# Performance work log

Hardware: AMD Instinct MI355X
Metric: run time of the kernel (lower is better)

## Reference

```python
import jax, jax.numpy as jnp
import numpy as np

DECAY = 0.95     # importance_decay
BUDGET = 1.0     # attention_budget
TOP_K = 10       # recall top_k used by get_context_embedding
EPS = 1e-8


def _gelu(x):
    # torch nn.GELU default = exact erf variant
    return jax.nn.gelu(x, approximate=False)


def setup_inputs() -> dict:
    key = jax.random.key(0)
    ks = jax.random.split(key, 8)
    B, N, D, H = 4096, 100, 4096, 128
    query = jax.random.normal(ks[0], (B, D), dtype=jnp.float32)
    seg_emb = jax.random.normal(ks[1], (N, D), dtype=jnp.float32)
    positions = jnp.arange(N, dtype=jnp.int32)
    s1 = 1.0 / np.sqrt(D)
    s2 = 1.0 / np.sqrt(H)
    iw1 = jax.random.normal(ks[2], (D, H), dtype=jnp.float32) * s1
    ib1 = jnp.zeros((H,), dtype=jnp.float32)
    iw2 = jax.random.normal(ks[3], (H, 1), dtype=jnp.float32) * s2
    ib2 = jnp.zeros((1,), dtype=jnp.float32)
    rw1 = jax.random.normal(ks[4], (2 * D, H), dtype=jnp.float32) * (1.0 / np.sqrt(2 * D))
    rb1 = jnp.zeros((H,), dtype=jnp.float32)
    rw2 = jax.random.normal(ks[5], (H, 1), dtype=jnp.float32) * s2
    rb2 = jnp.zeros((1,), dtype=jnp.float32)
    return {"query": query, "seg_emb": seg_emb, "positions": positions,
            "iw1": iw1, "ib1": ib1, "iw2": iw2, "ib2": ib2,
            "rw1": rw1, "rb1": rb1, "rw2": rw2, "rb2": rb2}


def reference(query, seg_emb, positions, iw1, ib1, iw2, ib2, rw1, rb1, rw2, rb2):
    # query: [B, D], seg_emb: [N, D]
    B, D = query.shape
    N = seg_emb.shape[0]

    # importance_scorer per segment: Linear->GELU->Linear->Sigmoid, [N]
    importance = jax.nn.sigmoid(_gelu(seg_emb @ iw1 + ib1) @ iw2 + ib2)[:, 0]

    # relevance_scorer on concat([query, seg]); split rw1 to avoid [B,N,2D] concat
    qh = query @ rw1[:D]            # [B, H]
    sh = seg_emb @ rw1[D:]          # [N, H]
    h = _gelu(qh[:, None, :] + sh[None, :, :] + rb1)   # [B, N, H]
    rel = jax.nn.sigmoid(jnp.einsum('bnh,ho->bn', h, rw2) + rb2[0])  # [B, N]

    # recall score: importance * relevance * (0.5 + 0.5 * decay^(N - pos - 1))
    pos_factor = DECAY ** (N - positions.astype(jnp.float32) - 1.0)  # [N]
    score = importance[None, :] * rel * (0.5 + 0.5 * pos_factor[None, :])

    _, topi = jax.lax.top_k(score, TOP_K)               # [B, K]

    sel_rel = jnp.take_along_axis(rel, topi, axis=1)    # [B, K]
    sel_imp = importance[topi]                          # [B, K]
    w = sel_imp * sel_rel
    w = w / (jnp.sum(w, axis=-1, keepdims=True) + EPS) * BUDGET

    sel_emb = seg_emb[topi]                             # [B, K, D]
    context = jnp.einsum('bk,bkd->bd', w, sel_emb)      # [B, D]
    return query + context
```

## Files before the change

kernel.cpp:

```cpp
#include <hip/hip_runtime.h>
#include <math.h>

#define DDIM 4096
#define NSEG 100
#define HDIM 128
#define BROWS 4096
#define TOPK 10
#define KSLICES 8

typedef __attribute__((ext_vector_type(8))) short bf16x8;
typedef __attribute__((ext_vector_type(4))) float f32x4;

__device__ __forceinline__ void gl16(const void* g, void* l) {
    __builtin_amdgcn_global_load_lds(
        (const __attribute__((address_space(1))) unsigned int*)g,
        (__attribute__((address_space(3))) unsigned int*)l,
        16, 0, 0);
}

__device__ __forceinline__ float gelu_f(float x) {
    float u  = x * 0.70710678118654752440f;
    float au = fminf(fabsf(u), 3.9f);
    float t  = __builtin_amdgcn_rcpf(fmaf(0.3275911f, au, 1.0f));
    float p  = fmaf(fmaf(fmaf(fmaf(1.061405429f, t, -1.453152027f), t,
                              1.421413741f), t, -0.284496736f), t, 0.254829592f) * t;
    float e  = __expf(-au * au);
    float er = fmaf(-p, e, 1.0f);
    er = copysignf(er, u);
    return 0.5f * x * (1.0f + er);
}

__device__ __forceinline__ void split8(const float4& a, const float4& b,
                                       bf16x8& hi, bf16x8& lo) {
    float v[8] = {a.x, a.y, a.z, a.w, b.x, b.y, b.z, b.w};
    uint hw[4], lw[4];
    #pragma unroll
    for (int j = 0; j < 4; ++j) {
        uint u0 = __float_as_uint(v[2 * j]);
        uint u1 = __float_as_uint(v[2 * j + 1]);
        hw[j] = (u0 >> 16) | (u1 & 0xffff0000u);
        float r0 = v[2 * j]     - __uint_as_float(u0 & 0xffff0000u);
        float r1 = v[2 * j + 1] - __uint_as_float(u1 & 0xffff0000u);
        lw[j] = (__float_as_uint(r0) >> 16) | (__float_as_uint(r1) & 0xffff0000u);
    }
    uint4 h = make_uint4(hw[0], hw[1], hw[2], hw[3]);
    uint4 l = make_uint4(lw[0], lw[1], lw[2], lw[3]);
    hi = __builtin_bit_cast(bf16x8, h);
    lo = __builtin_bit_cast(bf16x8, l);
}

__global__ void k_front(const float* __restrict__ seg,
                        const float* __restrict__ iw1,
                        const float* __restrict__ rw1,
                        float* __restrict__ segp,
                        unsigned char* __restrict__ btI) {
    __shared__ __align__(16) float shf[32 * 129];
    int bid = blockIdx.x, tid = threadIdx.x;
    if (bid < 1600) {
        float (*segT)[5] = reinterpret_cast<float (*)[5]>(shf);
        int ng = bid % 25;
        int ks = (bid / 25) * 64;
        {
            int k = tid & 63, j = tid >> 6;
            segT[k][j] = seg[(size_t)(ng * 4 + j) * DDIM + ks + k];
        }
        __syncthreads();
        int col = tid;
        float a0 = 0.f, a1 = 0.f, a2 = 0.f, a3 = 0.f;
        const float* w = (col < HDIM) ? (iw1 + col)
                                      : (rw1 + (size_t)DDIM * HDIM + (col - HDIM));
        #pragma unroll 8
        for (int k = 0; k < 64; ++k) {
            float wv = w[(size_t)(ks + k) * HDIM];
            a0 = fmaf(segT[k][0], wv, a0);
            a1 = fmaf(segT[k][1], wv, a1);
            a2 = fmaf(segT[k][2], wv, a2);
            a3 = fmaf(segT[k][3], wv, a3);
        }
        float* outp = segp + (size_t)(bid / 25) * (NSEG * 256) + (size_t)(ng * 4) * 256 + col;
        outp[0] = a0; outp[256] = a1; outp[512] = a2; outp[768] = a3;
    } else {
        float (*tile)[129] = reinterpret_cast<float (*)[129]>(shf);
        int c = bid - 1600;
        #pragma unroll
        for (int i = 0; i < 4; ++i) {
            int e = i * 1024 + tid * 4;
            int k = e >> 7, n = e & 127;
            *reinterpret_cast<float4*>(&tile[k][n]) =
                *reinterpret_cast<const float4*>(rw1 + (size_t)(c * 32 + k) * HDIM + n);
        }
        __syncthreads();
        unsigned char* img = btI + (size_t)c * 16384;
        #pragma unroll
        for (int uu = 0; uu < 2; ++uu) {
            int U = tid * 2 + uu;
            int col = U >> 2;
            int u = U & 3;
            int Z = (col * 64 + u * 16) ^ ((col & 7) << 4);
            uint hw[4], lw[4];
            #pragma unroll
            for (int j = 0; j < 4; ++j) {
                float x0 = tile[u * 8 + 2 * j][col];
                float x1 = tile[u * 8 + 2 * j + 1][col];
                uint u0 = __float_as_uint(x0), u1 = __float_as_uint(x1);
                hw[j] = (u0 >> 16) | (u1 & 0xffff0000u);
                float r0 = x0 - __uint_as_float(u0 & 0xffff0000u);
                float r1 = x1 - __uint_as_float(u1 & 0xffff0000u);
                lw[j] = (__float_as_uint(r0) >> 16) | (__float_as_uint(r1) & 0xffff0000u);
            }
            *reinterpret_cast<uint4*>(img + Z)        = make_uint4(hw[0], hw[1], hw[2], hw[3]);
            *reinterpret_cast<uint4*>(img + 8192 + Z) = make_uint4(lw[0], lw[1], lw[2], lw[3]);
        }
    }
}

__global__ __launch_bounds__(256)
void k_mid(const float* __restrict__ query,
           const unsigned char* __restrict__ btI,
           float* __restrict__ qhp,
           const float* __restrict__ segp,
           const int* __restrict__ positions,
           const float* __restrict__ ib1,
           const float* __restrict__ iw2,
           const float* __restrict__ ib2,
           const float* __restrict__ rb1,
           float* __restrict__ shwT, float* __restrict__ impA,
           float* __restrict__ cA) {
    __shared__ __align__(16) char lds[49152];
    int bid = blockIdx.x, tid = threadIdx.x;
    if (bid < 512) {
        float  (*Ab)[2048] = reinterpret_cast<float (*)[2048]>(lds);
        ushort (*Bb)[8192] = reinterpret_cast<ushort (*)[8192]>(lds + 16384);
        int lane = tid & 63, w = tid >> 6;
        int cl = lane & 15, rg = lane >> 4;
        int wm = w >> 1, wn = w & 1;
        int m0 = (bid & 63) * 64;
        int ky = bid >> 6;
        int k0 = ky * 512;

        const float* aSrc0;
        const float* aSrc1;
        {
            int X0 = w * 2048 + lane * 16;
            int r0_ = X0 >> 7, kb0 = (X0 & 127) ^ ((r0_ & 7) << 4);
            aSrc0 = query + (size_t)(m0 + r0_) * DDIM + k0 + (kb0 >> 2);
            int X1 = X0 + 1024;
            int r1_ = X1 >> 7, kb1 = (X1 & 127) ^ ((r1_ & 7) << 4);
            aSrc1 = query + (size_t)(m0 + r1_) * DDIM + k0 + (kb1 >> 2);
        }
        const unsigned char* bSrc = btI + (size_t)(ky * 16) * 16384 + w * 4096 + lane * 16;

        f32x4 acc[2][4];
        #pragma unroll
        for (int mi = 0; mi < 2; ++mi)
            #pragma unroll
            for (int nf = 0; nf < 4; ++nf) acc[mi][nf] = (f32x4)0.f;

        {
            char* ad = (char*)&Ab[0][0] + w * 2048;
            char* bd = (char*)&Bb[0][0] + w * 4096;
            gl16(aSrc0, ad);
            gl16(aSrc1, ad + 1024);
            #pragma unroll
            for (int j = 0; j < 4; ++j) gl16(bSrc + j * 1024, bd + j * 1024);
        }
        __syncthreads();

        #pragma unroll 2
        for (int t = 0; t < 16; ++t) {
            int cur = t & 1;
            if (t < 15) {
                char* ad = (char*)&Ab[cur ^ 1][0] + w * 2048;
                char* bd = (char*)&Bb[cur ^ 1][0] + w * 4096;
                gl16(aSrc0 + (t + 1) * 32, ad);
                gl16(aSrc1 + (t + 1) * 32, ad + 1024);
                const unsigned char* bs = bSrc + (size_t)(t + 1) * 16384;
                #pragma unroll
                for (int j = 0; j < 4; ++j) gl16(bs + j * 1024, bd + j * 1024);
            }
            bf16x8 ah[2], al[2];
            #pragma unroll
            for (int mi = 0; mi < 2; ++mi) {
                int row = wm * 32 + mi * 16 + cl;
                int sw = (row & 7) << 4;
                int Sb = row * 128 + rg * 32;
                float4 f0 = *reinterpret_cast<const float4*>((const char*)&Ab[cur][0] + (Sb ^ sw));
                float4 f1 = *reinterpret_cast<const float4*>((const char*)&Ab[cur][0] + ((Sb + 16) ^ sw));
                split8(f0, f1, ah[mi], al[mi]);
            }
            #pragma unroll
            for (int nf = 0; nf < 4; ++nf) {
                int col = wn * 64 + nf * 16 + cl;
                int Z = (col * 64 + rg * 16) ^ ((col & 7) << 4);
                bf16x8 bh = *reinterpret_cast<const bf16x8*>((const char*)&Bb[cur][0] + Z);
                bf16x8 bl = *reinterpret_cast<const bf16x8*>((const char*)&Bb[cur][0] + 8192 + Z);
                #pragma unroll
                for (int mi = 0; mi < 2; ++mi) {
                    acc[mi][nf] = __builtin_amdgcn_mfma_f32_16x16x32_bf16(ah[mi], bh, acc[mi][nf], 0, 0, 0);
                    acc[mi][nf] = __builtin_amdgcn_mfma_f32_16x16x32_bf16(al[mi], bh, acc[mi][nf], 0, 0, 0);
                    acc[mi][nf] = __builtin_amdgcn_mfma_f32_16x16x32_bf16(ah[mi], bl, acc[mi][nf], 0, 0, 0);
                }
            }
            __syncthreads();
        }

        float* op = qhp + (size_t)ky * (BROWS * HDIM);
        #pragma unroll
        for (int mi = 0; mi < 2; ++mi) {
            int rowb = m0 + wm * 32 + mi * 16 + rg * 4;
            #pragma unroll
            for (int nf = 0; nf < 4; ++nf) {
                int col = wn * 64 + nf * 16 + cl;
                #pragma unroll
                for (int r = 0; r < 4; ++r)
                    op[(size_t)(rowb + r) * HDIM + col] = acc[mi][nf][r];
            }
        }
    } else {
        float* red = reinterpret_cast<float*>(lds);
        int n = bid - 512;
        float v = 0.f;
        #pragma unroll
        for (int s = 0; s < 64; ++s)
            v += segp[(size_t)s * (NSEG * 256) + (size_t)n * 256 + tid];
        if (tid < HDIM) {
            red[tid] = gelu_f(v + ib1[tid]) * iw2[tid];
        } else {
            shwT[(size_t)(tid - HDIM) * NSEG + n] = v + rb1[tid - HDIM];
        }
        __syncthreads();
        if (tid == 0) {
            float s = 0.f;
            for (int j = 0; j < HDIM; ++j) s += red[j];
            float imp = 1.f / (1.f + expf(-(s + ib2[0])));
            float pf = powf(0.95f, (float)NSEG - (float)positions[n] - 1.0f);
            impA[n] = imp;
            cA[n] = imp * (0.5f + 0.5f * pf);
        }
    }
}

__global__ __launch_bounds__(256)
void k_relg(const float* __restrict__ qhp,
            const float* __restrict__ shwT,
            const float* __restrict__ rw2,
            const float* __restrict__ rb2,
            const float* __restrict__ impA,
            const float* __restrict__ cA,
            const float* __restrict__ query,
            const float* __restrict__ seg,
            float* __restrict__ out) {
    __shared__ float qs[2][HDIM];
    __shared__ float scL[2][128], wiL[2][128];
    __shared__ float wnS[2][TOPK];
    __shared__ int   idxS[2][TOPK];
    int tid = threadIdx.x;
    int b0 = blockIdx.x * 2;
    int g = tid >> 7, n = tid & 127;

    {
        size_t o = (size_t)(b0 + g) * HDIM + n;
        float v = qhp[o];
        #pragma unroll
        for (int s = 1; s < KSLICES; ++s)
            v += qhp[(size_t)s * (BROWS * HDIM) + o];
        qs[g][n] = v;
    }
    __syncthreads();

    int nn = (n < NSEG) ? n : (NSEG - 1);
    float a0 = 0.f;
    #pragma unroll 2
    for (int h = 0; h < HDIM; ++h) {
        float s = shwT[h * NSEG + nn];
        float w = rw2[h];
        a0 = fmaf(gelu_f(qs[g][h] + s), w, a0);
    }
    if (n < NSEG) {
        float rel = 1.f / (1.f + expf(-(a0 + rb2[0])));
        scL[g][n] = cA[n] * rel;
        wiL[g][n] = impA[n] * rel;
    }
    __syncthreads();

    int w = tid >> 6, lane = tid & 63;
    if (w < 2) {
        int rr = w;
        float s1 = scL[rr][lane];
        float w1 = wiL[rr][lane];
        int i2 = lane + 64;
        float s2 = (i2 < NSEG) ? scL[rr][i2] : -1e30f;
        float w2 = (i2 < NSEG) ? wiL[rr][i2] : 0.f;

        float wv[TOPK]; int idxv[TOPK]; float wsum = 0.f;
        #pragma unroll
        for (int k = 0; k < TOPK; ++k) {
            float s; int i;
            if (s2 > s1) { s = s2; i = i2; } else { s = s1; i = lane; }
            #pragma unroll
            for (int off = 1; off < 64; off <<= 1) {
                float os = __shfl_xor(s, off);
                int oi = __shfl_xor(i, off);
                if (os > s || (os == s && oi < i)) { s = os; i = oi; }
            }
            float wi = __shfl((i < 64) ? w1 : w2, i & 63);
            idxv[k] = i; wv[k] = wi; wsum += wi;
            if (i == lane) s1 = -1e30f;
            if (i == i2)   s2 = -1e30f;
        }
        if (lane == 0) {
            float denom = wsum + 1e-8f;
            #pragma unroll
            for (int k = 0; k < TOPK; ++k) {
                idxS[rr][k] = idxv[k];
                wnS[rr][k]  = wv[k] / denom;
            }
        }
    }
    __syncthreads();

    #pragma unroll
    for (int r = 0; r < 2; ++r) {
        int b = b0 + r;
        float wn_[TOPK]; const float* srow[TOPK];
        #pragma unroll
        for (int k = 0; k < TOPK; ++k) {
            wn_[k]  = wnS[r][k];
            srow[k] = seg + (size_t)idxS[r][k] * DDIM;
        }
        const float* qrow = query + (size_t)b * DDIM;
        float* orow = out + (size_t)b * DDIM;
        #pragma unroll
        for (int c = 0; c < 4; ++c) {
            int d0 = c * 1024 + tid * 4;
            float4 q4 = *reinterpret_cast<const float4*>(qrow + d0);
            #pragma unroll
            for (int k = 0; k < TOPK; ++k) {
                float4 s4 = *reinterpret_cast<const float4*>(srow[k] + d0);
                q4.x = fmaf(wn_[k], s4.x, q4.x);
                q4.y = fmaf(wn_[k], s4.y, q4.y);
                q4.z = fmaf(wn_[k], s4.z, q4.z);
                q4.w = fmaf(wn_[k], s4.w, q4.w);
            }
            *reinterpret_cast<float4*>(orow + d0) = q4;
        }
    }
}

extern "C" void kernel_launch(void* const* d_in, const int* in_sizes, int n_in,
                              void* d_out, int out_size, void* d_ws, size_t ws_size,
                              hipStream_t stream) {
    const float* query = (const float*)d_in[0];
    const float* seg   = (const float*)d_in[1];
    const int*   pos   = (const int*)d_in[2];
    const float* iw1   = (const float*)d_in[3];
    const float* ib1   = (const float*)d_in[4];
    const float* iw2   = (const float*)d_in[5];
    const float* ib2   = (const float*)d_in[6];
    const float* rw1   = (const float*)d_in[7];
    const float* rb1   = (const float*)d_in[8];
    const float* rw2   = (const float*)d_in[9];
    const float* rb2   = (const float*)d_in[10];
    float* out = (float*)d_out;

    char* ws = (char*)d_ws;
    float* qhp  = (float*)(ws);
    float* segp = (float*)(ws + 16 * 1024 * 1024);
    unsigned char* btI = (unsigned char*)(ws + 23 * 1024 * 1024);
    float* shwT = (float*)(ws + 25 * 1024 * 1024);
    float* impA = (float*)(ws + 25 * 1024 * 1024 + 64 * 1024);
    float* cA   = (float*)(ws + 25 * 1024 * 1024 + 64 * 1024 + 4096);

    hipLaunchKernelGGL(k_front, dim3(1728), dim3(256), 0, stream,
                       seg, iw1, rw1, segp, btI);
    hipLaunchKernelGGL(k_mid, dim3(612), dim3(256), 0, stream,
                       query, btI, qhp, segp, pos, ib1, iw2, ib2, rb1,
                       shwT, impA, cA);
    hipLaunchKernelGGL(k_relg, dim3(BROWS / 2), dim3(256), 0, stream,
                       qhp, shwT, rw2, rb2, impA, cA, query, seg, out);
}
```

Baseline: 125.0 us.

## Split relevance/top-k and gather into separate kernels with more rows per block

The fused relevance+topk+gather kernel is split in two. The relevance kernel now handles 4 rows per block, each thread computes two rows sharing the shwT loads, and all four waves run top-k. It writes indices and normalized weights to workspace. A new gather kernel uses one block per row and issues all four float4 query loads plus per-k segment loads up front to get more memory-level parallelism. This adds a kernel launch and a small workspace round trip.

```diff
diff --git a/kernel.cpp b/kernel.cpp
--- a/kernel.cpp
+++ b/kernel.cpp
@@ -241,50 +241,55 @@
 }
 
 __global__ __launch_bounds__(256)
-void k_relg(const float* __restrict__ qhp,
-            const float* __restrict__ shwT,
-            const float* __restrict__ rw2,
-            const float* __restrict__ rb2,
-            const float* __restrict__ impA,
-            const float* __restrict__ cA,
-            const float* __restrict__ query,
-            const float* __restrict__ seg,
-            float* __restrict__ out) {
-    __shared__ float qs[2][HDIM];
-    __shared__ float scL[2][128], wiL[2][128];
-    __shared__ float wnS[2][TOPK];
-    __shared__ int   idxS[2][TOPK];
+void k_rel(const float* __restrict__ qhp,
+           const float* __restrict__ shwT,
+           const float* __restrict__ rw2,
+           const float* __restrict__ rb2,
+           const float* __restrict__ impA,
+           const float* __restrict__ cA,
+           int* __restrict__ idxA,
+           float* __restrict__ wnA) {
+    __shared__ float qs[4][HDIM];
+    __shared__ float scL[4][128], wiL[4][128];
     int tid = threadIdx.x;
-    int b0 = blockIdx.x * 2;
-    int g = tid >> 7, n = tid & 127;
-
-    {
-        size_t o = (size_t)(b0 + g) * HDIM + n;
+    int b0 = blockIdx.x * 4;
+
+    #pragma unroll
+    for (int i = 0; i < 2; ++i) {
+        int idx = tid + i * 256;
+        int r = idx >> 7, h = idx & 127;
+        size_t o = (size_t)(b0 + r) * HDIM + h;
         float v = qhp[o];
         #pragma unroll
         for (int s = 1; s < KSLICES; ++s)
             v += qhp[(size_t)s * (BROWS * HDIM) + o];
-        qs[g][n] = v;
+        qs[r][h] = v;
     }
     __syncthreads();
 
+    int g = tid >> 7, n = tid & 127;
     int nn = (n < NSEG) ? n : (NSEG - 1);
-    float a0 = 0.f;
+    int r0 = g * 2;
+    float a0 = 0.f, a1 = 0.f;
     #pragma unroll 2
     for (int h = 0; h < HDIM; ++h) {
         float s = shwT[h * NSEG + nn];
         float w = rw2[h];
-        a0 = fmaf(gelu_f(qs[g][h] + s), w, a0);
+        a0 = fmaf(gelu_f(qs[r0 + 0][h] + s), w, a0);
+        a1 = fmaf(gelu_f(qs[r0 + 1][h] + s), w, a1);
     }
     if (n < NSEG) {
-        float rel = 1.f / (1.f + expf(-(a0 + rb2[0])));
-        scL[g][n] = cA[n] * rel;
-        wiL[g][n] = impA[n] * rel;
+        float rb2f = rb2[0];
+        float ca = cA[n], ia = impA[n];
+        float rel0 = 1.f / (1.f + expf(-(a0 + rb2f)));
+        float rel1 = 1.f / (1.f + expf(-(a1 + rb2f)));
+        scL[r0 + 0][n] = ca * rel0;  wiL[r0 + 0][n] = ia * rel0;
+        scL[r0 + 1][n] = ca * rel1;  wiL[r0 + 1][n] = ia * rel1;
     }
     __syncthreads();
 
     int w = tid >> 6, lane = tid & 63;
-    if (w < 2) {
+    {
         int rr = w;
         float s1 = scL[rr][lane];
         float w1 = wiL[rr][lane];
@@ -309,42 +314,55 @@
             if (i == i2)   s2 = -1e30f;
         }
         if (lane == 0) {
+            int b = b0 + rr;
             float denom = wsum + 1e-8f;
             #pragma unroll
             for (int k = 0; k < TOPK; ++k) {
-                idxS[rr][k] = idxv[k];
-                wnS[rr][k]  = wv[k] / denom;
-            }
-        }
-    }
-    __syncthreads();
-
-    #pragma unroll
-    for (int r = 0; r < 2; ++r) {
-        int b = b0 + r;
-        float wn_[TOPK]; const float* srow[TOPK];
-        #pragma unroll
-        for (int k = 0; k < TOPK; ++k) {
-            wn_[k]  = wnS[r][k];
-            srow[k] = seg + (size_t)idxS[r][k] * DDIM;
-        }
-        const float* qrow = query + (size_t)b * DDIM;
-        float* orow = out + (size_t)b * DDIM;
+                idxA[b * TOPK + k] = idxv[k];
+                wnA[b * TOPK + k]  = wv[k] / denom;
+            }
+        }
+    }
+}
+
+__global__ void k_gather(const float* __restrict__ query,
+                         const float* __restrict__ seg,
+                         const int* __restrict__ idxA,
+                         const float* __restrict__ wnA,
+                         float* __restrict__ out) {
+    int b = blockIdx.x, tid = threadIdx.x;
+    const int*   ip = idxA + b * TOPK;
+    const float* wp = wnA  + b * TOPK;
+    float wn[TOPK]; const float* srow[TOPK];
+    #pragma unroll
+    for (int k = 0; k < TOPK; ++k) {
+        wn[k]   = wp[k];
+        srow[k] = seg + (size_t)ip[k] * DDIM;
+    }
+    const float* qrow = query + (size_t)b * DDIM;
+    float* orow = out + (size_t)b * DDIM;
+
+    float4 q[4];
+    #pragma unroll
+    for (int c = 0; c < 4; ++c)
+        q[c] = *reinterpret_cast<const float4*>(qrow + c * 1024 + tid * 4);
+    #pragma unroll
+    for (int k = 0; k < TOPK; ++k) {
+        float4 s[4];
+        #pragma unroll
+        for (int c = 0; c < 4; ++c)
+            s[c] = *reinterpret_cast<const float4*>(srow[k] + c * 1024 + tid * 4);
         #pragma unroll
         for (int c = 0; c < 4; ++c) {
-            int d0 = c * 1024 + tid * 4;
-            float4 q4 = *reinterpret_cast<const float4*>(qrow + d0);
-            #pragma unroll
-            for (int k = 0; k < TOPK; ++k) {
-                float4 s4 = *reinterpret_cast<const float4*>(srow[k] + d0);
-                q4.x = fmaf(wn_[k], s4.x, q4.x);
-                q4.y = fmaf(wn_[k], s4.y, q4.y);
-                q4.z = fmaf(wn_[k], s4.z, q4.z);
-                q4.w = fmaf(wn_[k], s4.w, q4.w);
-            }
-            *reinterpret_cast<float4*>(orow + d0) = q4;
-        }
-    }
+            q[c].x = fmaf(wn[k], s[c].x, q[c].x);
+            q[c].y = fmaf(wn[k], s[c].y, q[c].y);
+            q[c].z = fmaf(wn[k], s[c].z, q[c].z);
+            q[c].w = fmaf(wn[k], s[c].w, q[c].w);
+        }
+    }
+    #pragma unroll
+    for (int c = 0; c < 4; ++c)
+        *reinterpret_cast<float4*>(orow + c * 1024 + tid * 4) = q[c];
 }
 
 extern "C" void kernel_launch(void* const* d_in, const int* in_sizes, int n_in,
@@ -370,12 +388,16 @@
     float* shwT = (float*)(ws + 25 * 1024 * 1024);
     float* impA = (float*)(ws + 25 * 1024 * 1024 + 64 * 1024);
     float* cA   = (float*)(ws + 25 * 1024 * 1024 + 64 * 1024 + 4096);
+    int*   idxA = (int*)  (ws + 25 * 1024 * 1024 + 128 * 1024);
+    float* wnA  = (float*)(ws + 25 * 1024 * 1024 + 320 * 1024);
 
     hipLaunchKernelGGL(k_front, dim3(1728), dim3(256), 0, stream,
                        seg, iw1, rw1, segp, btI);
     hipLaunchKernelGGL(k_mid, dim3(612), dim3(256), 0, stream,
                        query, btI, qhp, segp, pos, ib1, iw2, ib2, rb1,
                        shwT, impA, cA);
-    hipLaunchKernelGGL(k_relg, dim3(BROWS / 2), dim3(256), 0, stream,
-                       qhp, shwT, rw2, rb2, impA, cA, query, seg, out);
-}
+    hipLaunchKernelGGL(k_rel, dim3(BROWS / 4), dim3(256), 0, stream,
+                       qhp, shwT, rw2, rb2, impA, cA, idxA, wnA);
+    hipLaunchKernelGGL(k_gather, dim3(BROWS), dim3(256), 0, stream,
+                       query, seg, idxA, wnA, out);
+}
```

Result: faster. 115.3 us (-7.8%).
